# Performance work log

Measured on AMD Instinct MI355X. Metric: run time of the kernel, lower is better.

## Reference

```python
import jax, jax.numpy as jnp
import numpy as np

N_NODES = 100000
N_EDGES = 1600000
NUM_RELS = 8
NUM_BASES = 8
E_DIM = 32
MAX_LEN = 8
H_DIM = 64
OUT_DIM = 64


def setup_inputs() -> dict:
    key = jax.random.key(0)
    ks = jax.random.split(key, 16)
    inp = {
        'feat': jax.random.randint(ks[0], (N_NODES, MAX_LEN), 0, N_NODES, dtype=jnp.int32),
        'src': jax.random.randint(ks[1], (N_EDGES,), 0, N_NODES, dtype=jnp.int32),
        'dst': jax.random.randint(ks[2], (N_EDGES,), 0, N_NODES, dtype=jnp.int32),
        'etype': jax.random.randint(ks[3], (N_EDGES,), 0, NUM_RELS, dtype=jnp.int32),
        'norm': jax.random.uniform(ks[4], (N_EDGES, 1), dtype=jnp.float32),
        'emb_w': jax.random.normal(ks[5], (N_NODES, E_DIM), dtype=jnp.float32),
        'sm_w': jax.random.normal(ks[6], (H_DIM, E_DIM * MAX_LEN), dtype=jnp.float32) * 0.06,
        'sm_b': jax.random.normal(ks[7], (H_DIM,), dtype=jnp.float32) * 0.02,
        'V1': jax.random.normal(ks[8], (NUM_BASES, H_DIM, H_DIM), dtype=jnp.float32) * 0.12,
        'comp1': jax.random.normal(ks[9], (NUM_RELS, NUM_BASES), dtype=jnp.float32) * 0.35,
        'b1': jax.random.normal(ks[10], (H_DIM,), dtype=jnp.float32) * 0.02,
        'V2': jax.random.normal(ks[11], (NUM_BASES, H_DIM, OUT_DIM), dtype=jnp.float32) * 0.12,
        'comp2': jax.random.normal(ks[12], (NUM_RELS, NUM_BASES), dtype=jnp.float32) * 0.35,
        'b2': jax.random.normal(ks[13], (OUT_DIM,), dtype=jnp.float32) * 0.02,
    }
    return inp


def _rel_graph_conv(x, src, dst, etype, norm, V, comp, bias, num_nodes):
    # basis decomposition: W_r = sum_b comp[r,b] * V[b]  -> [R, in, out]
    W = jnp.einsum('rb,bio->rio', comp, V)
    # transform all node feats under every relation (R small) -> [R, N, out]
    H = jnp.einsum('ni,rio->rno', x, W)
    # per-edge relation-typed gather of transformed source features
    msg = H[etype, src] * norm            # [E, out]
    agg = jax.ops.segment_sum(msg, dst, num_segments=num_nodes)  # [N, out]
    return agg + bias


def reference(feat, src, dst, etype, norm, emb_w, sm_w, sm_b,
              V1, comp1, b1, V2, comp2, b2):
    n = feat.shape[0]
    # embedding lookup [N, max_len, e_dim] -> flatten -> linear size_matcher
    nf = emb_w[feat].reshape(n, -1)
    x = nf @ sm_w.T + sm_b                # [N, h_dim]
    h = _rel_graph_conv(x, src, dst, etype, norm, V1, comp1, b1, n)
    h = jax.nn.relu(h)                    # dropout p=0.0 -> identity
    out = _rel_graph_conv(h, src, dst, etype, norm, V2, comp2, b2, n)
    return out
```

## Files before the change

### kernel.cpp

```cpp
#include <hip/hip_runtime.h>

#define N_NODES 100000
#define N_PAD 100032
#define N_EDGES 1600000
#define NUM_RELS 8
#define KDIM 256
#define HD 64
#define KF 512

#define B_SHIFT 8
#define NBUCK 392
#define NBUCK_USED 391
#define NBLK_P 512
#define TPB_P 256
#define EPB 3125

typedef __attribute__((ext_vector_type(8))) short bf16x8;
typedef __attribute__((ext_vector_type(4))) float f32x4;

struct EP { int x, y; };
typedef const __attribute__((address_space(4))) EP*  ep_cptr;
typedef const __attribute__((address_space(4))) int* ci_cptr;

__device__ inline unsigned short f2bf(float f) {
    unsigned u = __float_as_uint(f);
    u += 0x7fff + ((u >> 16) & 1);
    return (unsigned short)(u >> 16);
}
__device__ inline float bf2f(unsigned short s) {
    return __uint_as_float(((unsigned)s) << 16);
}
__device__ inline unsigned packtrunc(float x, float y) {
    return (__float_as_uint(x) >> 16) | (__float_as_uint(y) & 0xffff0000u);
}

__global__ void k_weights(const float* __restrict__ V1, const float* __restrict__ comp1,
                          const float* __restrict__ V2, const float* __restrict__ comp2,
                          const float* __restrict__ sm_w,
                          unsigned short* __restrict__ WpF1, unsigned short* __restrict__ WpF2,
                          unsigned short* __restrict__ smPack) {
    int idx = blockIdx.x * 256 + threadIdx.x;
    if (idx < 2 * NUM_RELS * 64 * 64) {
        int l = idx >> 15;
        int r = (idx >> 12) & 7;
        int k = (idx >> 6) & 63;
        int o = idx & 63;
        const float* V = l ? V2 : V1;
        const float* comp = l ? comp2 : comp1;
        float s = 0.f;
#pragma unroll
        for (int b = 0; b < 8; b++) s += comp[r * 8 + b] * V[(b * 64 + k) * 64 + o];
        int kk = r * 64 + k;
        int ss = kk >> 5, q = (kk >> 3) & 3, j = kk & 7;
        unsigned short* Wp = l ? WpF2 : WpF1;
        Wp[(((ss * 4 + q) * 64) + o) * 8 + j] = f2bf(s);
    } else {
        int j = idx - 65536;
        if (j < KDIM * HD) {
            int k = j >> 6, o = j & 63;
            int s = k >> 5, q = (k >> 3) & 3, jj = k & 7;
            smPack[(((s * 4 + q) * 64) + o) * 8 + jj] = f2bf(sm_w[o * KDIM + k]);
        }
    }
}

__launch_bounds__(TPB_P)
__global__ void k_pcount(const int* __restrict__ dst, int* __restrict__ cnt) {
    __shared__ int lh[NBUCK];
    int t = threadIdx.x, blk = blockIdx.x;
    for (int b = t; b < NBUCK; b += TPB_P) lh[b] = 0;
    __syncthreads();
    int base = blk * EPB;
    for (int i = t; i < EPB; i += TPB_P) atomicAdd(&lh[dst[base + i] >> B_SHIFT], 1);
    __syncthreads();
    for (int b = t; b < NBUCK; b += TPB_P) cnt[blk * NBUCK + b] = lh[b];
}

__launch_bounds__(NBLK_P)
__global__ void k_pscan(const int* __restrict__ cnt, int* __restrict__ boffm, int* __restrict__ btot) {
    __shared__ int s[NBLK_P];
    int b = blockIdx.x, t = threadIdx.x;
    int v = cnt[t * NBUCK + b];
    s[t] = v;
    __syncthreads();
    for (int off = 1; off < NBLK_P; off <<= 1) {
        int u = (t >= off) ? s[t - off] : 0;
        __syncthreads();
        s[t] += u;
        __syncthreads();
    }
    boffm[t * NBUCK + b] = s[t] - v;
    if (t == NBLK_P - 1) btot[b] = s[NBLK_P - 1];
}

__launch_bounds__(512)
__global__ void k_bscan(const int* __restrict__ btot, int* __restrict__ bstart, int* __restrict__ rowptr8) {
    __shared__ int s[512];
    int t = threadIdx.x;
    int v = (t < NBUCK_USED) ? btot[t] : 0;
    s[t] = v;
    __syncthreads();
    for (int off = 1; off < 512; off <<= 1) {
        int u = (t >= off) ? s[t - off] : 0;
        __syncthreads();
        s[t] += u;
        __syncthreads();
    }
    bstart[t] = s[t] - v;
    if (t == 0) rowptr8[(size_t)N_NODES * 8] = N_EDGES;
}

__launch_bounds__(TPB_P)
__global__ void k_pscatter(const int* __restrict__ src, const int* __restrict__ dst,
                           const int* __restrict__ et, const float* __restrict__ norm,
                           const int* __restrict__ boffm, const int* __restrict__ bstart,
                           int2* __restrict__ staged) {
    __shared__ int ldsoff[NBUCK];
    int t = threadIdx.x, blk = blockIdx.x;
    for (int b = t; b < NBUCK; b += TPB_P) ldsoff[b] = bstart[b] + boffm[blk * NBUCK + b];
    __syncthreads();
    int base = blk * EPB;
    for (int i = t; i < EPB; i += TPB_P) {
        int e = base + i;
        int d = dst[e];
        int bu = d >> B_SHIFT;
        int pos = atomicAdd(&ldsoff[bu], 1);
        int packed = src[e] | (et[e] << 17) | ((d & 255) << 20);
        staged[pos] = make_int2(packed, __float_as_int(norm[e]));
    }
}

__launch_bounds__(512)
__global__ void k_finalize(const int2* __restrict__ staged, const int* __restrict__ bstart,
                           const int* __restrict__ btot, int* __restrict__ rowptr8,
                           int2* __restrict__ edata) {
    __shared__ int lh[2048];
    __shared__ int s512[512];
    __shared__ int lsc[2048];
    int b = blockIdx.x, t = threadIdx.x;
    int base = bstart[b];
    int cnt = btot[b];
    lh[t] = 0; lh[t + 512] = 0; lh[t + 1024] = 0; lh[t + 1536] = 0;
    __syncthreads();
    int2 held[9];
    int key[9], rank[9];
    int nh = 0;
    for (int i = t; i < cnt; i += 512) {
        int2 ed = staged[base + i];
        int k = (ed.x >> 17) & 2047;
        held[nh] = ed; key[nh] = k; rank[nh] = atomicAdd(&lh[k], 1); nh++;
    }
    __syncthreads();
    int b0 = lh[t * 4], b1 = lh[t * 4 + 1], b2 = lh[t * 4 + 2], b3 = lh[t * 4 + 3];
    int tot = b0 + b1 + b2 + b3;
    s512[t] = tot;
    __syncthreads();
    for (int off = 1; off < 512; off <<= 1) {
        int u = (t >= off) ? s512[t - off] : 0;
        __syncthreads();
        s512[t] += u;
        __syncthreads();
    }
    int excl = s512[t] - tot;
    lsc[t * 4] = excl;
    lsc[t * 4 + 1] = excl + b0;
    lsc[t * 4 + 2] = excl + b0 + b1;
    lsc[t * 4 + 3] = excl + b0 + b1 + b2;
    __syncthreads();
    int limit = (N_NODES << 3) - (b << 11);
    for (int idx = t; idx < 2048; idx += 512)
        if (idx < limit) rowptr8[(b << 11) + idx] = base + lsc[idx];
    for (int i = 0; i < nh; i++) {
        int p = base + lsc[key[i]] + rank[i];
        int srcv = held[i].x & 0x1FFFF;
        int etv  = (held[i].x >> 17) & 7;
        edata[p] = make_int2((srcv << 7) | etv, held[i].y);
    }
}

__launch_bounds__(256)
__global__ void k_sizematch(const int* __restrict__ feat, const float* __restrict__ emb_w,
                            const unsigned short* __restrict__ smPack, const float* __restrict__ sm_b,
                            unsigned short* __restrict__ xb) {
    int t = threadIdx.x;
    int wave = t >> 6, lane = t & 63;
    int q = lane >> 4, c = lane & 15;
    int n0 = blockIdx.x * 64 + wave * 16;
    int node = n0 + c;
    int nclamp = (node < N_NODES) ? node : (N_NODES - 1);
    const int4* fr = (const int4*)(feat + (size_t)nclamp * 8);
    int4 f0 = fr[0], f1 = fr[1];
    int fidx[8] = {f0.x, f0.y, f0.z, f0.w, f1.x, f1.y, f1.z, f1.w};
    f32x4 acc[4];
#pragma unroll
    for (int i = 0; i < 4; i++) acc[i] = (f32x4){0.f, 0.f, 0.f, 0.f};
    const bf16x8* B8 = (const bf16x8*)smPack;
#pragma unroll
    for (int s = 0; s < 8; s++) {
        const float4* ar = (const float4*)(emb_w + (size_t)fidx[s] * 32 + q * 8);
        float4 a0 = ar[0], a1 = ar[1];
        union { unsigned u[4]; bf16x8 v; } A;
        A.u[0] = packtrunc(a0.x, a0.y);
        A.u[1] = packtrunc(a0.z, a0.w);
        A.u[2] = packtrunc(a1.x, a1.y);
        A.u[3] = packtrunc(a1.z, a1.w);
#pragma unroll
        for (int tl = 0; tl < 4; tl++) {
            bf16x8 b = B8[(s * 4 + q) * 64 + tl * 16 + c];
            acc[tl] = __builtin_amdgcn_mfma_f32_16x16x32_bf16(A.v, b, acc[tl], 0, 0, 0);
        }
    }
    int row_base = n0 + q * 4;
    bool full = (n0 + 15 < N_NODES);
#pragma unroll
    for (int tl = 0; tl < 4; tl++) {
        int o = tl * 16 + c;
        float bia = sm_b[o];
#pragma unroll
        for (int r = 0; r < 4; r++) {
            int nd = row_base + r;
            if (full || nd < N_NODES)
                xb[(size_t)nd * 64 + o] = f2bf(acc[tl][r] + bia);
        }
    }
}

__launch_bounds__(256)
__global__ void k_fused(const unsigned short* __restrict__ xin,
                        const int* __restrict__ rowptr8, const int2* __restrict__ edata,
                        const unsigned short* __restrict__ WpF, const float* __restrict__ bias,
                        float* __restrict__ outf, unsigned short* __restrict__ outb, int mode) {
    __shared__ __align__(16) unsigned short agg[16 * 520];
    int t = threadIdx.x;
    int wave = t >> 6, lane = t & 63;
    int n0 = blockIdx.x * 16;
    ep_cptr ep4 = (ep_cptr)(unsigned long long)edata;
    ci_cptr rp4 = (ci_cptr)(unsigned long long)rowptr8;
    {
        int* a4 = (int*)agg + wave * 4 * 260;
        for (int i = lane; i < 4 * 260; i += 64) a4[i] = 0;
    }
#define EF(S,k)  int x##S##k = ep4[j##S + (k)].x, y##S##k = ep4[j##S + (k)].y;
#define EFM(S,k) int q##S##k = j##S + (k); \
                 int c##S##k = (q##S##k <= last##S) ? q##S##k : last##S; \
                 c##S##k = (c##S##k < 0) ? 0 : c##S##k; \
                 int x##S##k = ep4[c##S##k].x; \
                 int y##S##k = (q##S##k <= last##S) ? ep4[c##S##k].y : 0;
#define GF(S,k)  unsigned short w##S##k = *((const unsigned short*)((const char*)xin + (x##S##k & 0x00FFFF80)) + lane);
#define CN(S,k)  { int et = x##S##k & 7; \
                   float keep = (et == prev##S) ? 1.0f : 0.0f; \
                   prev##S = et; \
                   acc##S = fmaf(__int_as_float(y##S##k), bf2f(w##S##k), acc##S * keep); \
                   unsigned bb = __float_as_uint(acc##S) + 0x8000u; \
                   aggrow##S[et * 64 + lane] = (unsigned short)(bb >> 16); }
#define EF8(S)   EF(S,0) EF(S,1) EF(S,2) EF(S,3) EF(S,4) EF(S,5) EF(S,6) EF(S,7)
#define EFM8(S)  EFM(S,0) EFM(S,1) EFM(S,2) EFM(S,3) EFM(S,4) EFM(S,5) EFM(S,6) EFM(S,7)
#define GF8(S)   GF(S,0) GF(S,1) GF(S,2) GF(S,3) GF(S,4) GF(S,5) GF(S,6) GF(S,7)
#define CN8(S)   CN(S,0) CN(S,1) CN(S,2) CN(S,3) CN(S,4) CN(S,5) CN(S,6) CN(S,7)
    for (int np = 0; np < 2; np++) {
        int lrowA = wave * 4 + np * 2;
        int lrowB = lrowA + 1;
        int nA = __builtin_amdgcn_readfirstlane(n0 + lrowA);
        int nB = nA + 1;
        int j0A = rp4[(size_t)nA * 8], j1A = rp4[(size_t)nA * 8 + 8];
        int j0B = rp4[(size_t)nB * 8], j1B = rp4[(size_t)nB * 8 + 8];
        unsigned short* aggrowA = agg + lrowA * 520;
        unsigned short* aggrowB = agg + lrowB * 520;
        float accA = 0.f, accB = 0.f;
        int prevA = -1, prevB = -1;
        int jA = j0A, jB = j0B;
        while (jA + 8 <= j1A && jB + 8 <= j1B) {
            EF8(A) EF8(B) GF8(A) GF8(B) CN8(A) CN8(B)
            jA += 8; jB += 8;
        }
        while (jA + 8 <= j1A) { EF8(A) GF8(A) CN8(A) jA += 8; }
        while (jB + 8 <= j1B) { EF8(B) GF8(B) CN8(B) jB += 8; }
        {
            int lastA = j1A - 1, lastB = j1B - 1;
            if (((j1A - jA) | (j1B - jB)) > 0) {
                EFM8(A) EFM8(B) GF8(A) GF8(B) CN8(A) CN8(B)
            }
        }
    }
#undef EF
#undef EFM
#undef GF
#undef CN
#undef EF8
#undef EFM8
#undef GF8
#undef CN8
    __syncthreads();
    int q = lane >> 4, c = lane & 15;
    int o16 = wave * 16;
    f32x4 accd = (f32x4){0.f, 0.f, 0.f, 0.f};
    const bf16x8* B8 = (const bf16x8*)WpF;
#pragma unroll
    for (int s = 0; s < 16; s++) {
        bf16x8 a = *(const bf16x8*)&agg[c * 520 + s * 32 + q * 8];
        bf16x8 bfr = B8[(s * 4 + q) * 64 + o16 + c];
        accd = __builtin_amdgcn_mfma_f32_16x16x32_bf16(a, bfr, accd, 0, 0, 0);
    }
    int col = o16 + c;
    float bia = bias[col];
#pragma unroll
    for (int r = 0; r < 4; r++) {
        int node = n0 + q * 4 + r;
        float v = accd[r] + bia;
        if (mode == 1) {
            v = fmaxf(v, 0.f);
            outb[(size_t)node * 64 + col] = f2bf(v);
        } else {
            outf[(size_t)node * 64 + col] = v;
        }
    }
}

extern "C" void kernel_launch(void* const* d_in, const int* in_sizes, int n_in,
                              void* d_out, int out_size, void* d_ws, size_t ws_size,
                              hipStream_t stream) {
    const int*   feat  = (const int*)d_in[0];
    const int*   src   = (const int*)d_in[1];
    const int*   dst   = (const int*)d_in[2];
    const int*   etype = (const int*)d_in[3];
    const float* norm  = (const float*)d_in[4];
    const float* emb_w = (const float*)d_in[5];
    const float* sm_w  = (const float*)d_in[6];
    const float* sm_b  = (const float*)d_in[7];
    const float* V1    = (const float*)d_in[8];
    const float* comp1 = (const float*)d_in[9];
    const float* b1    = (const float*)d_in[10];
    const float* V2    = (const float*)d_in[11];
    const float* comp2 = (const float*)d_in[12];
    const float* b2    = (const float*)d_in[13];
    float* out = (float*)d_out;

    char* p = (char*)d_ws;
    auto alloc = [&](size_t bytes) { void* q = (void*)p; p += (bytes + 255) & ~(size_t)255; return q; };
    unsigned short* xb   = (unsigned short*)alloc((size_t)N_PAD * 64 * 2);
    unsigned short* hb   = (unsigned short*)alloc((size_t)N_PAD * 64 * 2);
    unsigned short* WpF1 = (unsigned short*)alloc((size_t)KF * HD * 2);
    unsigned short* WpF2 = (unsigned short*)alloc((size_t)KF * HD * 2);
    unsigned short* smPack = (unsigned short*)alloc(KDIM * HD * 2);
    int*   cnt    = (int*)alloc((size_t)NBLK_P * NBUCK * 4);
    int*   boffm  = (int*)alloc((size_t)NBLK_P * NBUCK * 4);
    int*   btot   = (int*)alloc((size_t)NBUCK * 4);
    int*   bstart = (int*)alloc((size_t)(NBUCK + 1) * 4);
    int*   rowptr8 = (int*)alloc(((size_t)N_NODES * 8 + 1) * 4);
    int2*  staged = (int2*)alloc((size_t)N_EDGES * 8);
    int2*  edata  = (int2*)alloc((size_t)N_EDGES * 8);

    k_weights<<<320, 256, 0, stream>>>(V1, comp1, V2, comp2, sm_w, WpF1, WpF2, smPack);

    k_pcount<<<NBLK_P, TPB_P, 0, stream>>>(dst, cnt);
    k_pscan<<<NBUCK_USED, NBLK_P, 0, stream>>>(cnt, boffm, btot);
    k_bscan<<<1, 512, 0, stream>>>(btot, bstart, rowptr8);
    k_pscatter<<<NBLK_P, TPB_P, 0, stream>>>(src, dst, etype, norm, boffm, bstart, staged);
    k_finalize<<<NBUCK_USED, 512, 0, stream>>>(staged, bstart, btot, rowptr8, edata);

    k_sizematch<<<N_PAD / 64, 256, 0, stream>>>(feat, emb_w, smPack, sm_b, xb);

    k_fused<<<N_NODES / 16, 256, 0, stream>>>(xb, rowptr8, edata, WpF1, b1, nullptr, hb, 1);
    k_fused<<<N_NODES / 16, 256, 0, stream>>>(hb, rowptr8, edata, WpF2, b2, out, nullptr, 0);
}
```

Before: 299.8 us.

## Replace bucketed two-pass edge sort with global atomic counting sort per (dst,rel)

Replaces the LDS-bucketed partition and finalize sort with a direct global histogram over 800k (dst,rel) bins, a three-kernel scan, and an atomic scatter into CSR order. The histogram is fused into a single prep kernel that also builds the weights and converts the embedding table to bf16 (now round-to-nearest instead of truncation), so the size-matcher gathers half the bytes. This drops the staging buffer and one pass over the edges, but relies on global atomics that contend more and scatter writes that land in random order, which loses the locality the old bucket scheme had.

```diff
diff --git a/kernel.cpp b/kernel.cpp
--- a/kernel.cpp
+++ b/kernel.cpp
@@ -8,12 +8,8 @@
 #define HD 64
 #define KF 512
 
-#define B_SHIFT 8
-#define NBUCK 392
-#define NBUCK_USED 391
-#define NBLK_P 512
-#define TPB_P 256
-#define EPB 3125
+#define NBINS 800000
+#define NSB1 782
 
 typedef __attribute__((ext_vector_type(8))) short bf16x8;
 typedef __attribute__((ext_vector_type(4))) float f32x4;
@@ -30,17 +26,17 @@
 __device__ inline float bf2f(unsigned short s) {
     return __uint_as_float(((unsigned)s) << 16);
 }
-__device__ inline unsigned packtrunc(float x, float y) {
-    return (__float_as_uint(x) >> 16) | (__float_as_uint(y) & 0xffff0000u);
-}
-
-__global__ void k_weights(const float* __restrict__ V1, const float* __restrict__ comp1,
-                          const float* __restrict__ V2, const float* __restrict__ comp2,
-                          const float* __restrict__ sm_w,
-                          unsigned short* __restrict__ WpF1, unsigned short* __restrict__ WpF2,
-                          unsigned short* __restrict__ smPack) {
+
+__launch_bounds__(256)
+__global__ void k_prep(const float* __restrict__ V1, const float* __restrict__ comp1,
+                       const float* __restrict__ V2, const float* __restrict__ comp2,
+                       const float* __restrict__ sm_w, const float* __restrict__ emb_w,
+                       const int* __restrict__ dst, const int* __restrict__ et,
+                       unsigned short* __restrict__ WpF1, unsigned short* __restrict__ WpF2,
+                       unsigned short* __restrict__ smPack,
+                       unsigned* __restrict__ emb_bf, int* __restrict__ cnt8) {
     int idx = blockIdx.x * 256 + threadIdx.x;
-    if (idx < 2 * NUM_RELS * 64 * 64) {
+    if (idx < 65536) {
         int l = idx >> 15;
         int r = (idx >> 12) & 7;
         int k = (idx >> 6) & 63;
@@ -54,132 +50,81 @@
         int ss = kk >> 5, q = (kk >> 3) & 3, j = kk & 7;
         unsigned short* Wp = l ? WpF2 : WpF1;
         Wp[(((ss * 4 + q) * 64) + o) * 8 + j] = f2bf(s);
+    } else if (idx < 81920) {
+        int j = idx - 65536;
+        int k = j >> 6, o = j & 63;
+        int s = k >> 5, q = (k >> 3) & 3, jj = k & 7;
+        smPack[(((s * 4 + q) * 64) + o) * 8 + jj] = f2bf(sm_w[o * KDIM + k]);
+    } else if (idx < 81920 + 1600000) {
+        int j = idx - 81920;
+        const float2* f2p = (const float2*)emb_w;
+        float2 f = f2p[j];
+        emb_bf[j] = ((unsigned)f2bf(f.x)) | (((unsigned)f2bf(f.y)) << 16);
     } else {
-        int j = idx - 65536;
-        if (j < KDIM * HD) {
-            int k = j >> 6, o = j & 63;
-            int s = k >> 5, q = (k >> 3) & 3, jj = k & 7;
-            smPack[(((s * 4 + q) * 64) + o) * 8 + jj] = f2bf(sm_w[o * KDIM + k]);
-        }
-    }
-}
-
-__launch_bounds__(TPB_P)
-__global__ void k_pcount(const int* __restrict__ dst, int* __restrict__ cnt) {
-    __shared__ int lh[NBUCK];
+        int e = idx - 81920 - 1600000;
+        if (e < N_EDGES) atomicAdd(&cnt8[dst[e] * 8 + et[e]], 1);
+    }
+}
+
+__launch_bounds__(1024)
+__global__ void k_scan1(int* __restrict__ cnt8, int* __restrict__ btmp) {
+    __shared__ int s[1024];
     int t = threadIdx.x, blk = blockIdx.x;
-    for (int b = t; b < NBUCK; b += TPB_P) lh[b] = 0;
-    __syncthreads();
-    int base = blk * EPB;
-    for (int i = t; i < EPB; i += TPB_P) atomicAdd(&lh[dst[base + i] >> B_SHIFT], 1);
-    __syncthreads();
-    for (int b = t; b < NBUCK; b += TPB_P) cnt[blk * NBUCK + b] = lh[b];
-}
-
-__launch_bounds__(NBLK_P)
-__global__ void k_pscan(const int* __restrict__ cnt, int* __restrict__ boffm, int* __restrict__ btot) {
-    __shared__ int s[NBLK_P];
-    int b = blockIdx.x, t = threadIdx.x;
-    int v = cnt[t * NBUCK + b];
+    int i = blk * 1024 + t;
+    int v = (i < NBINS) ? cnt8[i] : 0;
     s[t] = v;
     __syncthreads();
-    for (int off = 1; off < NBLK_P; off <<= 1) {
+    for (int off = 1; off < 1024; off <<= 1) {
         int u = (t >= off) ? s[t - off] : 0;
         __syncthreads();
         s[t] += u;
         __syncthreads();
     }
-    boffm[t * NBUCK + b] = s[t] - v;
-    if (t == NBLK_P - 1) btot[b] = s[NBLK_P - 1];
-}
-
-__launch_bounds__(512)
-__global__ void k_bscan(const int* __restrict__ btot, int* __restrict__ bstart, int* __restrict__ rowptr8) {
-    __shared__ int s[512];
+    if (i < NBINS) cnt8[i] = s[t] - v;
+    if (t == 1023) btmp[blk] = s[1023];
+}
+
+__launch_bounds__(1024)
+__global__ void k_scan2(int* __restrict__ btmp) {
+    __shared__ int s[1024];
     int t = threadIdx.x;
-    int v = (t < NBUCK_USED) ? btot[t] : 0;
+    int v = (t < NSB1) ? btmp[t] : 0;
     s[t] = v;
     __syncthreads();
-    for (int off = 1; off < 512; off <<= 1) {
+    for (int off = 1; off < 1024; off <<= 1) {
         int u = (t >= off) ? s[t - off] : 0;
         __syncthreads();
         s[t] += u;
         __syncthreads();
     }
-    bstart[t] = s[t] - v;
-    if (t == 0) rowptr8[(size_t)N_NODES * 8] = N_EDGES;
-}
-
-__launch_bounds__(TPB_P)
-__global__ void k_pscatter(const int* __restrict__ src, const int* __restrict__ dst,
+    if (t < NSB1) btmp[t] = s[t] - v;
+}
+
+__launch_bounds__(1024)
+__global__ void k_scan3(const int* __restrict__ cnt8, const int* __restrict__ btmp,
+                        int* __restrict__ rowptr8, int* __restrict__ wpos) {
+    int t = threadIdx.x, blk = blockIdx.x;
+    int i = blk * 1024 + t;
+    if (i < NBINS) {
+        int val = cnt8[i] + btmp[blk];
+        rowptr8[i] = val;
+        wpos[i] = val;
+    }
+    if (i == 0) rowptr8[NBINS] = N_EDGES;
+}
+
+__launch_bounds__(256)
+__global__ void k_escatter(const int* __restrict__ src, const int* __restrict__ dst,
                            const int* __restrict__ et, const float* __restrict__ norm,
-                           const int* __restrict__ boffm, const int* __restrict__ bstart,
-                           int2* __restrict__ staged) {
-    __shared__ int ldsoff[NBUCK];
-    int t = threadIdx.x, blk = blockIdx.x;
-    for (int b = t; b < NBUCK; b += TPB_P) ldsoff[b] = bstart[b] + boffm[blk * NBUCK + b];
-    __syncthreads();
-    int base = blk * EPB;
-    for (int i = t; i < EPB; i += TPB_P) {
-        int e = base + i;
-        int d = dst[e];
-        int bu = d >> B_SHIFT;
-        int pos = atomicAdd(&ldsoff[bu], 1);
-        int packed = src[e] | (et[e] << 17) | ((d & 255) << 20);
-        staged[pos] = make_int2(packed, __float_as_int(norm[e]));
-    }
-}
-
-__launch_bounds__(512)
-__global__ void k_finalize(const int2* __restrict__ staged, const int* __restrict__ bstart,
-                           const int* __restrict__ btot, int* __restrict__ rowptr8,
-                           int2* __restrict__ edata) {
-    __shared__ int lh[2048];
-    __shared__ int s512[512];
-    __shared__ int lsc[2048];
-    int b = blockIdx.x, t = threadIdx.x;
-    int base = bstart[b];
-    int cnt = btot[b];
-    lh[t] = 0; lh[t + 512] = 0; lh[t + 1024] = 0; lh[t + 1536] = 0;
-    __syncthreads();
-    int2 held[9];
-    int key[9], rank[9];
-    int nh = 0;
-    for (int i = t; i < cnt; i += 512) {
-        int2 ed = staged[base + i];
-        int k = (ed.x >> 17) & 2047;
-        held[nh] = ed; key[nh] = k; rank[nh] = atomicAdd(&lh[k], 1); nh++;
-    }
-    __syncthreads();
-    int b0 = lh[t * 4], b1 = lh[t * 4 + 1], b2 = lh[t * 4 + 2], b3 = lh[t * 4 + 3];
-    int tot = b0 + b1 + b2 + b3;
-    s512[t] = tot;
-    __syncthreads();
-    for (int off = 1; off < 512; off <<= 1) {
-        int u = (t >= off) ? s512[t - off] : 0;
-        __syncthreads();
-        s512[t] += u;
-        __syncthreads();
-    }
-    int excl = s512[t] - tot;
-    lsc[t * 4] = excl;
-    lsc[t * 4 + 1] = excl + b0;
-    lsc[t * 4 + 2] = excl + b0 + b1;
-    lsc[t * 4 + 3] = excl + b0 + b1 + b2;
-    __syncthreads();
-    int limit = (N_NODES << 3) - (b << 11);
-    for (int idx = t; idx < 2048; idx += 512)
-        if (idx < limit) rowptr8[(b << 11) + idx] = base + lsc[idx];
-    for (int i = 0; i < nh; i++) {
-        int p = base + lsc[key[i]] + rank[i];
-        int srcv = held[i].x & 0x1FFFF;
-        int etv  = (held[i].x >> 17) & 7;
-        edata[p] = make_int2((srcv << 7) | etv, held[i].y);
-    }
+                           int* __restrict__ wpos, int2* __restrict__ edata) {
+    int e = blockIdx.x * 256 + threadIdx.x;
+    int d = dst[e], r = et[e];
+    int pos = atomicAdd(&wpos[d * 8 + r], 1);
+    edata[pos] = make_int2((src[e] << 7) | r, __float_as_int(norm[e]));
 }
 
 __launch_bounds__(256)
-__global__ void k_sizematch(const int* __restrict__ feat, const float* __restrict__ emb_w,
+__global__ void k_sizematch(const int* __restrict__ feat, const unsigned* __restrict__ emb_bf,
                             const unsigned short* __restrict__ smPack, const float* __restrict__ sm_b,
                             unsigned short* __restrict__ xb) {
     int t = threadIdx.x;
@@ -197,13 +142,9 @@
     const bf16x8* B8 = (const bf16x8*)smPack;
 #pragma unroll
     for (int s = 0; s < 8; s++) {
-        const float4* ar = (const float4*)(emb_w + (size_t)fidx[s] * 32 + q * 8);
-        float4 a0 = ar[0], a1 = ar[1];
-        union { unsigned u[4]; bf16x8 v; } A;
-        A.u[0] = packtrunc(a0.x, a0.y);
-        A.u[1] = packtrunc(a0.z, a0.w);
-        A.u[2] = packtrunc(a1.x, a1.y);
-        A.u[3] = packtrunc(a1.z, a1.w);
+        const int4* ar = (const int4*)((const char*)emb_bf + (size_t)fidx[s] * 64);
+        union { int4 i; bf16x8 v; } A;
+        A.i = ar[q];
 #pragma unroll
         for (int tl = 0; tl < 4; tl++) {
             bf16x8 b = B8[(s * 4 + q) * 64 + tl * 16 + c];
@@ -337,28 +278,28 @@
 
     char* p = (char*)d_ws;
     auto alloc = [&](size_t bytes) { void* q = (void*)p; p += (bytes + 255) & ~(size_t)255; return q; };
-    unsigned short* xb   = (unsigned short*)alloc((size_t)N_PAD * 64 * 2);
-    unsigned short* hb   = (unsigned short*)alloc((size_t)N_PAD * 64 * 2);
-    unsigned short* WpF1 = (unsigned short*)alloc((size_t)KF * HD * 2);
-    unsigned short* WpF2 = (unsigned short*)alloc((size_t)KF * HD * 2);
+    unsigned short* xb     = (unsigned short*)alloc((size_t)N_PAD * 64 * 2);
+    unsigned short* hb     = (unsigned short*)alloc((size_t)N_PAD * 64 * 2);
+    unsigned short* WpF1   = (unsigned short*)alloc((size_t)KF * HD * 2);
+    unsigned short* WpF2   = (unsigned short*)alloc((size_t)KF * HD * 2);
     unsigned short* smPack = (unsigned short*)alloc(KDIM * HD * 2);
-    int*   cnt    = (int*)alloc((size_t)NBLK_P * NBUCK * 4);
-    int*   boffm  = (int*)alloc((size_t)NBLK_P * NBUCK * 4);
-    int*   btot   = (int*)alloc((size_t)NBUCK * 4);
-    int*   bstart = (int*)alloc((size_t)(NBUCK + 1) * 4);
-    int*   rowptr8 = (int*)alloc(((size_t)N_NODES * 8 + 1) * 4);
-    int2*  staged = (int2*)alloc((size_t)N_EDGES * 8);
-    int2*  edata  = (int2*)alloc((size_t)N_EDGES * 8);
-
-    k_weights<<<320, 256, 0, stream>>>(V1, comp1, V2, comp2, sm_w, WpF1, WpF2, smPack);
-
-    k_pcount<<<NBLK_P, TPB_P, 0, stream>>>(dst, cnt);
-    k_pscan<<<NBUCK_USED, NBLK_P, 0, stream>>>(cnt, boffm, btot);
-    k_bscan<<<1, 512, 0, stream>>>(btot, bstart, rowptr8);
-    k_pscatter<<<NBLK_P, TPB_P, 0, stream>>>(src, dst, etype, norm, boffm, bstart, staged);
-    k_finalize<<<NBUCK_USED, 512, 0, stream>>>(staged, bstart, btot, rowptr8, edata);
-
-    k_sizematch<<<N_PAD / 64, 256, 0, stream>>>(feat, emb_w, smPack, sm_b, xb);
+    unsigned*       emb_bf = (unsigned*)alloc((size_t)N_NODES * 32 * 2);
+    int*   cnt8    = (int*)alloc((size_t)NBINS * 4);
+    int*   btmp    = (int*)alloc((size_t)1024 * 4);
+    int*   rowptr8 = (int*)alloc(((size_t)NBINS + 1) * 4);
+    int*   wpos    = (int*)alloc((size_t)NBINS * 4);
+    int2*  edata   = (int2*)alloc((size_t)N_EDGES * 8);
+
+    hipMemsetAsync(cnt8, 0, (size_t)NBINS * 4, stream);
+
+    k_prep<<<12820, 256, 0, stream>>>(V1, comp1, V2, comp2, sm_w, emb_w, dst, etype,
+                                      WpF1, WpF2, smPack, emb_bf, cnt8);
+    k_scan1<<<NSB1, 1024, 0, stream>>>(cnt8, btmp);
+    k_scan2<<<1, 1024, 0, stream>>>(btmp);
+    k_scan3<<<NSB1, 1024, 0, stream>>>(cnt8, btmp, rowptr8, wpos);
+    k_escatter<<<N_EDGES / 256, 256, 0, stream>>>(src, dst, etype, norm, wpos, edata);
+
+    k_sizematch<<<N_PAD / 64, 256, 0, stream>>>(feat, emb_bf, smPack, sm_b, xb);
 
     k_fused<<<N_NODES / 16, 256, 0, stream>>>(xb, rowptr8, edata, WpF1, b1, nullptr, hb, 1);
     k_fused<<<N_NODES / 16, 256, 0, stream>>>(hb, rowptr8, edata, WpF2, b2, out, nullptr, 0);
```

Result: slower. 409.9 us (+36.7%).
